# Kernel optimization log

Measured on AMD Instinct MI355X. Metric: run time of the kernel, lower is better.

## Reference

```python
import jax, jax.numpy as jnp
import numpy as np

N_NODES = 100_000
N_POS = 1_600_000
N_NEG = 1_600_000
HID = 32


def gcn_conv(x, edge_index, W, b, num_nodes):
    """torch_geometric GCNConv: add self-loops, symmetric norm, linear-first, bias after agg."""
    xl = x @ W  # [N, out]
    loops = jnp.arange(num_nodes, dtype=edge_index.dtype)
    src = jnp.concatenate([edge_index[0], loops])
    dst = jnp.concatenate([edge_index[1], loops])
    deg = jax.ops.segment_sum(jnp.ones_like(dst, dtype=xl.dtype), dst, num_segments=num_nodes)
    dinv = jnp.where(deg > 0, jax.lax.rsqrt(deg), 0.0)
    norm = dinv[src] * dinv[dst]  # [E+N]
    out = jax.ops.segment_sum(norm[:, None] * xl[src], dst, num_segments=num_nodes)
    return out + b


def setup_inputs() -> dict:
    key = jax.random.key(0)
    ks = jax.random.split(key, 8)
    x = jax.random.normal(ks[0], (N_NODES, HID), dtype=jnp.float32)
    pos_edge_index = jax.random.randint(ks[1], (2, N_POS), 0, N_NODES, dtype=jnp.int32)
    neg_edge_index = jax.random.randint(ks[2], (2, N_NEG), 0, N_NODES, dtype=jnp.int32)
    s = lambda fan_in: 1.0 / np.sqrt(fan_in)
    W1 = jax.random.normal(ks[3], (HID, 128), dtype=jnp.float32) * s(HID)
    b1 = jnp.zeros((128,), jnp.float32)
    W2 = jax.random.normal(ks[4], (128, HID), dtype=jnp.float32) * s(128)
    b2 = jnp.zeros((HID,), jnp.float32)
    Wm1 = jax.random.normal(ks[5], (2 * HID, HID), dtype=jnp.float32) * s(2 * HID)
    bm1 = jnp.zeros((HID,), jnp.float32)
    Wm2 = jax.random.normal(ks[6], (HID, 2), dtype=jnp.float32) * s(HID)
    bm2 = jnp.zeros((2,), jnp.float32)
    return dict(x=x, pos_edge_index=pos_edge_index, neg_edge_index=neg_edge_index,
                W1=W1, b1=b1, W2=W2, b2=b2, Wm1=Wm1, bm1=bm1, Wm2=Wm2, bm2=bm2)


def reference(x, pos_edge_index, neg_edge_index, W1, b1, W2, b2, Wm1, bm1, Wm2, bm2):
    n = x.shape[0]
    h = jax.nn.relu(gcn_conv(x, pos_edge_index, W1, b1, n))
    h = jax.nn.relu(gcn_conv(h, pos_edge_index, W2, b2, n))  # [N, hid]
    ei = jnp.concatenate([pos_edge_index, neg_edge_index], axis=-1)  # [2, Ep+En]
    feat = jnp.concatenate([h[ei[0]], h[ei[1]]], axis=1)  # [E, 2*hid]
    out = jax.nn.relu(feat @ Wm1 + bm1) @ Wm2 + bm2  # [E, 2]
    return out
```

## Files before the change

### kernel.cpp

```cpp
#include <hip/hip_runtime.h>
#include <hip/hip_fp16.h>


#define HIDN 32
#define SCAN_B 256

struct __align__(8) Half4 { __half2 a, b; };

__global__ void k_deg(const int* __restrict__ dst, int E, int N, int* __restrict__ deg8) {
    int e = blockIdx.x * blockDim.x + threadIdx.x;
    if (e < E)
        atomicAdd(&deg8[(size_t)(e & 7) * N + __builtin_nontemporal_load(dst + e)], 1);
}

__global__ void k_scan1(const int* __restrict__ deg8, int N,
                        int* __restrict__ part, int* __restrict__ bsum,
                        float* __restrict__ dinv,
                        const float4* __restrict__ x4, Half4* __restrict__ xs4) {
    __shared__ int sh[SCAN_B];
    __shared__ float dsh[SCAN_B];
    int t = threadIdx.x, i = blockIdx.x * SCAN_B + t;
    int v = 0;
    if (i < N) {
#pragma unroll
        for (int c = 0; c < 8; ++c) v += deg8[(size_t)c * N + i];
    }
    float dv = rsqrtf((float)(v + 1));
    if (i < N) dinv[i] = dv;
    dsh[t] = dv;
    sh[t] = v; __syncthreads();
    for (int o = 1; o < SCAN_B; o <<= 1) {
        int a = (t >= o) ? sh[t - o] : 0;
        __syncthreads();
        sh[t] += a;
        __syncthreads();
    }
    if (i < N) part[i] = sh[t] - v;
    if (t == SCAN_B - 1) bsum[blockIdx.x] = sh[t];
#pragma unroll
    for (int it = 0; it < 8; ++it) {
        int q = it * SCAN_B + t;
        int g = blockIdx.x * (SCAN_B * 8) + q;
        if (g < N * 8) {
            float w = dsh[q >> 3];
            float4 a = x4[g];
            Half4 hv;
            hv.a = __floats2half2_rn(a.x * w, a.y * w);
            hv.b = __floats2half2_rn(a.z * w, a.w * w);
            xs4[g] = hv;
        }
    }
}

__global__ void k_scan2(int* __restrict__ bsum, int nb) {
    __shared__ int sh[1024];
    int t = threadIdx.x;
    int v = (t < nb) ? bsum[t] : 0;
    sh[t] = v; __syncthreads();
    for (int o = 1; o < 1024; o <<= 1) {
        int a = (t >= o) ? sh[t - o] : 0;
        __syncthreads();
        sh[t] += a;
        __syncthreads();
    }
    if (t < nb) bsum[t] = sh[t] - v;
}

__global__ void k_scan3(const int* __restrict__ part, const int* __restrict__ bsum,
                        const int* __restrict__ deg8,
                        int N, int E, int* __restrict__ rowptr, int* __restrict__ cursor8) {
    int i = blockIdx.x * blockDim.x + threadIdx.x;
    if (i < N) {
        int r = part[i] + bsum[i / SCAN_B];
        rowptr[i] = r;
        int base = r;
#pragma unroll
        for (int c = 0; c < 8; ++c) {
            cursor8[(size_t)c * N + i] = base;
            base += deg8[(size_t)c * N + i];
        }
    }
    if (i == N) rowptr[N] = E;
}

__global__ void k_fill_sweep(const int* __restrict__ src, const int* __restrict__ dst,
                             int E, int N, int lo, int hi,
                             int* __restrict__ cursor8, int* __restrict__ csr) {
    int e = blockIdx.x * blockDim.x + threadIdx.x;
    if (e >= E) return;
    int d = __builtin_nontemporal_load(dst + e);
    if (d >= lo && d < hi) {
        int j = atomicAdd(&cursor8[(size_t)(e & 7) * N + d], 1);
        csr[j] = __builtin_nontemporal_load(src + e);
    }
}

#define ADD8(raw)                                        \
    {                                                    \
        const __half2* _h = (const __half2*)&(raw);      \
        float2 _f;                                       \
        _f = __half22float2(_h[0]); a0 += _f.x; a1 += _f.y; \
        _f = __half22float2(_h[1]); a2 += _f.x; a3 += _f.y; \
        _f = __half22float2(_h[2]); a4 += _f.x; a5 += _f.y; \
        _f = __half22float2(_h[3]); a6 += _f.x; a7 += _f.y; \
    }

__global__ void k_gather_h(const float4* __restrict__ tbl, const float* __restrict__ dinv,
                           const int* __restrict__ rowptr, const int* __restrict__ csr,
                           int N, float4* __restrict__ out) {
    int t = blockIdx.x * blockDim.x + threadIdx.x;
    if (t >= N * 4) return;
    int i = t >> 2, c = t & 3;
    float di = dinv[i];
    float a0 = 0.f, a1 = 0.f, a2 = 0.f, a3 = 0.f;
    float a4 = 0.f, a5 = 0.f, a6 = 0.f, a7 = 0.f;
    {
        float4 raw = tbl[(size_t)i * 4 + c];
        ADD8(raw);
    }
    int p = rowptr[i], end = rowptr[i + 1];
    for (; p + 3 < end; p += 4) {
        int s0 = __builtin_nontemporal_load(csr + p);
        int s1 = __builtin_nontemporal_load(csr + p + 1);
        int s2 = __builtin_nontemporal_load(csr + p + 2);
        int s3 = __builtin_nontemporal_load(csr + p + 3);
        float4 r0 = tbl[(size_t)s0 * 4 + c];
        float4 r1 = tbl[(size_t)s1 * 4 + c];
        float4 r2 = tbl[(size_t)s2 * 4 + c];
        float4 r3 = tbl[(size_t)s3 * 4 + c];
        ADD8(r0); ADD8(r1); ADD8(r2); ADD8(r3);
    }
    for (; p < end; ++p) {
        float4 r = tbl[(size_t)__builtin_nontemporal_load(csr + p) * 4 + c];
        ADD8(r);
    }
    out[(size_t)i * 8 + 2 * c]     = make_float4(a0 * di, a1 * di, a2 * di, a3 * di);
    out[(size_t)i * 8 + 2 * c + 1] = make_float4(a4 * di, a5 * di, a6 * di, a7 * di);
}

__global__ __launch_bounds__(256) void k_mlp1(
        const float4* __restrict__ agg1, const float* __restrict__ dinv,
        const float* __restrict__ W1, const float* __restrict__ b1,
        const float* __restrict__ W2, int N, __half* __restrict__ xl2s) {
    __shared__ float aT[32][65];
    __shared__ __half hT16[64][136];
    int t = threadIdx.x;
    int base = blockIdx.x * 64;
#pragma unroll
    for (int it = 0; it < 2; ++it) {
        int idx = it * 256 + t;
        int n = idx >> 3, q = idx & 7;
        int gi = base + n;
        float4 v = (gi < N) ? agg1[(size_t)gi * 8 + q] : make_float4(0.f, 0.f, 0.f, 0.f);
        aT[q * 4 + 0][n] = v.x; aT[q * 4 + 1][n] = v.y;
        aT[q * 4 + 2][n] = v.z; aT[q * 4 + 3][n] = v.w;
    }
    __syncthreads();
    int j = t & 31, r = t >> 5;
    int n0 = r * 8;
    float acc[8][4];
    {
        float4 bq = *reinterpret_cast<const float4*>(&b1[4 * j]);
#pragma unroll
        for (int n = 0; n < 8; ++n) {
            acc[n][0] = bq.x; acc[n][1] = bq.y; acc[n][2] = bq.z; acc[n][3] = bq.w;
        }
    }
#pragma unroll
    for (int k = 0; k < 32; ++k) {
        float4 w = *reinterpret_cast<const float4*>(&W1[k * 128 + 4 * j]);
#pragma unroll
        for (int n = 0; n < 8; ++n) {
            float a = aT[k][n0 + n];
            acc[n][0] = fmaf(a, w.x, acc[n][0]);
            acc[n][1] = fmaf(a, w.y, acc[n][1]);
            acc[n][2] = fmaf(a, w.z, acc[n][2]);
            acc[n][3] = fmaf(a, w.w, acc[n][3]);
        }
    }
#pragma unroll
    for (int n = 0; n < 8; ++n) {
        Half4 hv;
        hv.a = __floats2half2_rn(fmaxf(acc[n][0], 0.f), fmaxf(acc[n][1], 0.f));
        hv.b = __floats2half2_rn(fmaxf(acc[n][2], 0.f), fmaxf(acc[n][3], 0.f));
        *reinterpret_cast<Half4*>(&hT16[n0 + n][4 * j]) = hv;
    }
    __syncthreads();
    int jo = j & 7, ko = j >> 3;
    float acc2[8][4];
#pragma unroll
    for (int n = 0; n < 8; ++n) { acc2[n][0] = acc2[n][1] = acc2[n][2] = acc2[n][3] = 0.f; }
#pragma unroll
    for (int kk = 0; kk < 8; ++kk) {
        int kbase = ko * 32 + 4 * kk;
        float2 hf[8][2];
#pragma unroll
        for (int n = 0; n < 8; ++n) {
            Half4 hv = *reinterpret_cast<const Half4*>(&hT16[n0 + n][kbase]);
            hf[n][0] = __half22float2(hv.a);
            hf[n][1] = __half22float2(hv.b);
        }
#pragma unroll
        for (int c = 0; c < 4; ++c) {
            float4 w = *reinterpret_cast<const float4*>(&W2[(kbase + c) * 32 + 4 * jo]);
#pragma unroll
            for (int n = 0; n < 8; ++n) {
                float a = (c == 0) ? hf[n][0].x : (c == 1) ? hf[n][0].y
                        : (c == 2) ? hf[n][1].x : hf[n][1].y;
                acc2[n][0] = fmaf(a, w.x, acc2[n][0]);
                acc2[n][1] = fmaf(a, w.y, acc2[n][1]);
                acc2[n][2] = fmaf(a, w.z, acc2[n][2]);
                acc2[n][3] = fmaf(a, w.w, acc2[n][3]);
            }
        }
    }
#pragma unroll
    for (int n = 0; n < 8; ++n)
#pragma unroll
        for (int c = 0; c < 4; ++c) {
            acc2[n][c] += __shfl_xor(acc2[n][c], 8);
            acc2[n][c] += __shfl_xor(acc2[n][c], 16);
        }
    if (ko == 0) {
#pragma unroll
        for (int n = 0; n < 8; ++n) {
            int gi = base + n0 + n;
            if (gi < N) {
                float d = dinv[gi];
                Half4 hv;
                hv.a = __floats2half2_rn(acc2[n][0] * d, acc2[n][1] * d);
                hv.b = __floats2half2_rn(acc2[n][2] * d, acc2[n][3] * d);
                *reinterpret_cast<Half4*>(&xl2s[(size_t)gi * 32 + 4 * jo]) = hv;
            }
        }
    }
}

__global__ __launch_bounds__(256) void k_mlp2(
        const float4* __restrict__ agg2, const float* __restrict__ b2,
        const float* __restrict__ Wm1, int N,
        __half* __restrict__ gt, __half* __restrict__ gb) {
    __shared__ float hT[32][129];
    int t = threadIdx.x;
    int base = blockIdx.x * 128;
    const float4* b2q = reinterpret_cast<const float4*>(b2);
#pragma unroll
    for (int it = 0; it < 4; ++it) {
        int idx = it * 256 + t;
        int n = idx >> 3, q = idx & 7;
        int gi = base + n;
        float4 v = (gi < N) ? agg2[(size_t)gi * 8 + q] : make_float4(0.f, 0.f, 0.f, 0.f);
        float4 bb = b2q[q];
        hT[q * 4 + 0][n] = fmaxf(v.x + bb.x, 0.f);
        hT[q * 4 + 1][n] = fmaxf(v.y + bb.y, 0.f);
        hT[q * 4 + 2][n] = fmaxf(v.z + bb.z, 0.f);
        hT[q * 4 + 3][n] = fmaxf(v.w + bb.w, 0.f);
    }
    __syncthreads();
    int j = t & 15, r = t >> 4;
    int n0 = r * 8;
    int half = j >> 3, jo = j & 7;
    float acc[8][4];
#pragma unroll
    for (int n = 0; n < 8; ++n) { acc[n][0] = acc[n][1] = acc[n][2] = acc[n][3] = 0.f; }
#pragma unroll
    for (int k = 0; k < 32; ++k) {
        float4 w = *reinterpret_cast<const float4*>(&Wm1[(k + half * 32) * 32 + 4 * jo]);
#pragma unroll
        for (int n = 0; n < 8; ++n) {
            float a = hT[k][n0 + n];
            acc[n][0] = fmaf(a, w.x, acc[n][0]);
            acc[n][1] = fmaf(a, w.y, acc[n][1]);
            acc[n][2] = fmaf(a, w.z, acc[n][2]);
            acc[n][3] = fmaf(a, w.w, acc[n][3]);
        }
    }
    __half* dsttab = half ? gb : gt;
#pragma unroll
    for (int n = 0; n < 8; ++n) {
        int gi = base + n0 + n;
        if (gi < N) {
            Half4 hv;
            hv.a = __floats2half2_rn(acc[n][0], acc[n][1]);
            hv.b = __floats2half2_rn(acc[n][2], acc[n][3]);
            *reinterpret_cast<Half4*>(&dsttab[(size_t)gi * 32 + 4 * jo]) = hv;
        }
    }
}

__global__ void k_edge(const int* __restrict__ ps, const int* __restrict__ pd, int Ep,
                       const int* __restrict__ ns, const int* __restrict__ nd, int En,
                       int P,
                       const float4* __restrict__ gt4, const float4* __restrict__ gb4,
                       const float* __restrict__ bm1, const float* __restrict__ Wm2,
                       const float* __restrict__ bm2, float* __restrict__ out) {
    int t = blockIdx.x * blockDim.x + threadIdx.x;
    int p = t >> 2, q = t & 3;
    if (p >= P) return;
    int E = Ep + En;
    int e0 = p, e1 = p + P;
    int u0, v0;
    if (e0 < Ep) { u0 = __builtin_nontemporal_load(ps + e0); v0 = __builtin_nontemporal_load(pd + e0); }
    else         { u0 = __builtin_nontemporal_load(ns + (e0 - Ep)); v0 = __builtin_nontemporal_load(nd + (e0 - Ep)); }
    bool has1 = (e1 < E);
    int u1 = u0, v1 = v0;
    if (has1) {
        if (e1 < Ep) { u1 = __builtin_nontemporal_load(ps + e1); v1 = __builtin_nontemporal_load(pd + e1); }
        else         { u1 = __builtin_nontemporal_load(ns + (e1 - Ep)); v1 = __builtin_nontemporal_load(nd + (e1 - Ep)); }
    }
    float4 a0raw = gt4[(size_t)u0 * 4 + q];
    float4 b0raw = gb4[(size_t)v0 * 4 + q];
    float4 a1raw = gt4[(size_t)u1 * 4 + q];
    float4 b1raw = gb4[(size_t)v1 * 4 + q];
    const __half* a0h = (const __half*)&a0raw;
    const __half* b0h = (const __half*)&b0raw;
    const __half* a1h = (const __half*)&a1raw;
    const __half* b1h = (const __half*)&b1raw;
    int k0 = q * 8;
    float o00 = 0.f, o01 = 0.f, o10 = 0.f, o11 = 0.f;
#pragma unroll
    for (int r = 0; r < 8; ++r) {
        float bm = bm1[k0 + r];
        float w0 = Wm2[(k0 + r) * 2 + 0];
        float w1 = Wm2[(k0 + r) * 2 + 1];
        float h0 = fmaxf(__half2float(a0h[r]) + __half2float(b0h[r]) + bm, 0.f);
        o00 = fmaf(h0, w0, o00); o01 = fmaf(h0, w1, o01);
        float h1 = fmaxf(__half2float(a1h[r]) + __half2float(b1h[r]) + bm, 0.f);
        o10 = fmaf(h1, w0, o10); o11 = fmaf(h1, w1, o11);
    }
    o00 += __shfl_down(o00, 2, 4); o01 += __shfl_down(o01, 2, 4);
    o00 += __shfl_down(o00, 1, 4); o01 += __shfl_down(o01, 1, 4);
    o10 += __shfl_down(o10, 2, 4); o11 += __shfl_down(o11, 2, 4);
    o10 += __shfl_down(o10, 1, 4); o11 += __shfl_down(o11, 1, 4);
    if (q == 0) {
        float c0 = bm2[0], c1 = bm2[1];
        __builtin_nontemporal_store(o00 + c0, out + (size_t)e0 * 2 + 0);
        __builtin_nontemporal_store(o01 + c1, out + (size_t)e0 * 2 + 1);
        if (has1) {
            __builtin_nontemporal_store(o10 + c0, out + (size_t)e1 * 2 + 0);
            __builtin_nontemporal_store(o11 + c1, out + (size_t)e1 * 2 + 1);
        }
    }
}

extern "C" void kernel_launch(void* const* d_in, const int* in_sizes, int n_in,
                              void* d_out, int out_size, void* d_ws, size_t ws_size,
                              hipStream_t stream) {
    const float* x   = (const float*)d_in[0];
    const int*   pei = (const int*)d_in[1];
    const int*   nei = (const int*)d_in[2];
    const float* W1  = (const float*)d_in[3];
    const float* b1  = (const float*)d_in[4];
    const float* W2  = (const float*)d_in[5];
    const float* b2  = (const float*)d_in[6];
    const float* Wm1 = (const float*)d_in[7];
    const float* bm1 = (const float*)d_in[8];
    const float* Wm2 = (const float*)d_in[9];
    const float* bm2 = (const float*)d_in[10];

    const int N  = in_sizes[0] / HIDN;
    const int Ep = in_sizes[1] / 2;
    const int En = in_sizes[2] / 2;
    const int* ps = pei;
    const int* pd = pei + Ep;
    const int* ns = nei;
    const int* nd = nei + En;
    const int nb = (N + SCAN_B - 1) / SCAN_B;

    char* ws = (char*)d_ws;
    size_t off = 0;
    auto alloc = [&](size_t bytes) { size_t o = off; off += (bytes + 255) & ~(size_t)255; return o; };
    int*    deg8    = (int*)(ws + alloc((size_t)N * 8 * 4));
    int*    cursor8 = (int*)(ws + alloc((size_t)N * 8 * 4));
    float*  dinv    = (float*)(ws + alloc((size_t)N * 4));
    int*    part    = (int*)(ws + alloc((size_t)N * 4));
    int*    bsum    = (int*)(ws + alloc((size_t)1024 * 4));
    int*    rowptr  = (int*)(ws + alloc((size_t)(N + 1) * 4));
    int*    csr     = (int*)(ws + alloc((size_t)Ep * 4));
    __half* xs      = (__half*)(ws + alloc((size_t)N * HIDN * 2));
    float*  agg1    = (float*)(ws + alloc((size_t)N * HIDN * 4));
    __half* xl2s    = (__half*)(ws + alloc((size_t)N * HIDN * 2));
    float*  agg2    = (float*)(ws + alloc((size_t)N * HIDN * 4));
    __half* gt      = (__half*)(ws + alloc((size_t)N * HIDN * 2));
    __half* gb      = (__half*)(ws + alloc((size_t)N * HIDN * 2));

    hipMemsetAsync(deg8, 0, (size_t)N * 8 * 4, stream);
    k_deg<<<(Ep + 255) / 256, 256, 0, stream>>>(pd, Ep, N, deg8);
    k_scan1<<<nb, SCAN_B, 0, stream>>>(deg8, N, part, bsum, dinv,
                                       (const float4*)x, (Half4*)xs);
    k_scan2<<<1, 1024, 0, stream>>>(bsum, nb);
    k_scan3<<<(N + 256) / 256, 256, 0, stream>>>(part, bsum, deg8, N, Ep, rowptr, cursor8);
    {
        int grid = (Ep + 255) / 256;
        for (int s = 0; s < 4; ++s) {
            int lo = (int)((size_t)N * s / 4);
            int hi = (int)((size_t)N * (s + 1) / 4);
            k_fill_sweep<<<grid, 256, 0, stream>>>(ps, pd, Ep, N, lo, hi, cursor8, csr);
        }
    }

    k_gather_h<<<(N * 4 + 255) / 256, 256, 0, stream>>>(
        (const float4*)xs, dinv, rowptr, csr, N, (float4*)agg1);
    k_mlp1<<<(N + 63) / 64, 256, 0, stream>>>(
        (const float4*)agg1, dinv, W1, b1, W2, N, xl2s);

    k_gather_h<<<(N * 4 + 255) / 256, 256, 0, stream>>>(
        (const float4*)xl2s, dinv, rowptr, csr, N, (float4*)agg2);
    k_mlp2<<<(N + 127) / 128, 256, 0, stream>>>(
        (const float4*)agg2, b2, Wm1, N, gt, gb);

    {
        int E = Ep + En;
        int P = (E + 1) / 2;
        size_t threads = (size_t)P * 4;
        k_edge<<<(int)((threads + 255) / 256), 256, 0, stream>>>(
            ps, pd, Ep, ns, nd, En, P,
            (const float4*)gt, (const float4*)gb,
            bm1, Wm2, bm2, (float*)d_out);
    }
}
```

Before: 362.5 us.

## Fuse CSR gather into per-layer MLP kernels and split edge kernel in halves

The neighbor gather is folded into both dense layer kernels. Each block aggregates its 64 nodes directly into shared memory, so the fp32 agg1/agg2 intermediates are no longer written to and read back from global memory. The second layer's tile shrinks from 128 to 64 nodes so the gather maps one node per four threads. The edge MLP kernel is also launched as two half-range chunks. This removes two launches and about 25 MB of global traffic per layer. In exchange, the irregular gather now shares a block with the FMA work, which may cost occupancy and latency hiding.

```diff
diff --git a/kernel.cpp b/kernel.cpp
--- a/kernel.cpp
+++ b/kernel.cpp
@@ -105,55 +105,50 @@
         _f = __half22float2(_h[3]); a6 += _f.x; a7 += _f.y; \
     }
 
-__global__ void k_gather_h(const float4* __restrict__ tbl, const float* __restrict__ dinv,
-                           const int* __restrict__ rowptr, const int* __restrict__ csr,
-                           int N, float4* __restrict__ out) {
-    int t = blockIdx.x * blockDim.x + threadIdx.x;
-    if (t >= N * 4) return;
-    int i = t >> 2, c = t & 3;
-    float di = dinv[i];
-    float a0 = 0.f, a1 = 0.f, a2 = 0.f, a3 = 0.f;
-    float a4 = 0.f, a5 = 0.f, a6 = 0.f, a7 = 0.f;
-    {
-        float4 raw = tbl[(size_t)i * 4 + c];
-        ADD8(raw);
-    }
-    int p = rowptr[i], end = rowptr[i + 1];
-    for (; p + 3 < end; p += 4) {
-        int s0 = __builtin_nontemporal_load(csr + p);
-        int s1 = __builtin_nontemporal_load(csr + p + 1);
-        int s2 = __builtin_nontemporal_load(csr + p + 2);
-        int s3 = __builtin_nontemporal_load(csr + p + 3);
-        float4 r0 = tbl[(size_t)s0 * 4 + c];
-        float4 r1 = tbl[(size_t)s1 * 4 + c];
-        float4 r2 = tbl[(size_t)s2 * 4 + c];
-        float4 r3 = tbl[(size_t)s3 * 4 + c];
-        ADD8(r0); ADD8(r1); ADD8(r2); ADD8(r3);
-    }
-    for (; p < end; ++p) {
-        float4 r = tbl[(size_t)__builtin_nontemporal_load(csr + p) * 4 + c];
-        ADD8(r);
-    }
-    out[(size_t)i * 8 + 2 * c]     = make_float4(a0 * di, a1 * di, a2 * di, a3 * di);
-    out[(size_t)i * 8 + 2 * c + 1] = make_float4(a4 * di, a5 * di, a6 * di, a7 * di);
-}
-
-__global__ __launch_bounds__(256) void k_mlp1(
-        const float4* __restrict__ agg1, const float* __restrict__ dinv,
+__global__ __launch_bounds__(256) void k_l1(
+        const float4* __restrict__ xs, const float* __restrict__ dinv,
+        const int* __restrict__ rowptr, const int* __restrict__ csr,
         const float* __restrict__ W1, const float* __restrict__ b1,
         const float* __restrict__ W2, int N, __half* __restrict__ xl2s) {
     __shared__ float aT[32][65];
     __shared__ __half hT16[64][136];
     int t = threadIdx.x;
     int base = blockIdx.x * 64;
-#pragma unroll
-    for (int it = 0; it < 2; ++it) {
-        int idx = it * 256 + t;
-        int n = idx >> 3, q = idx & 7;
+    {
+        int n = t >> 2, c = t & 3;
         int gi = base + n;
-        float4 v = (gi < N) ? agg1[(size_t)gi * 8 + q] : make_float4(0.f, 0.f, 0.f, 0.f);
-        aT[q * 4 + 0][n] = v.x; aT[q * 4 + 1][n] = v.y;
-        aT[q * 4 + 2][n] = v.z; aT[q * 4 + 3][n] = v.w;
+        float a0 = 0.f, a1 = 0.f, a2 = 0.f, a3 = 0.f;
+        float a4 = 0.f, a5 = 0.f, a6 = 0.f, a7 = 0.f;
+        if (gi < N) {
+            float di = dinv[gi];
+            {
+                float4 raw = xs[(size_t)gi * 4 + c];
+                ADD8(raw);
+            }
+            int p = rowptr[gi], end = rowptr[gi + 1];
+            for (; p + 3 < end; p += 4) {
+                int s0 = __builtin_nontemporal_load(csr + p);
+                int s1 = __builtin_nontemporal_load(csr + p + 1);
+                int s2 = __builtin_nontemporal_load(csr + p + 2);
+                int s3 = __builtin_nontemporal_load(csr + p + 3);
+                float4 r0 = xs[(size_t)s0 * 4 + c];
+                float4 r1 = xs[(size_t)s1 * 4 + c];
+                float4 r2 = xs[(size_t)s2 * 4 + c];
+                float4 r3 = xs[(size_t)s3 * 4 + c];
+                ADD8(r0); ADD8(r1); ADD8(r2); ADD8(r3);
+            }
+            for (; p < end; ++p) {
+                float4 rr = xs[(size_t)__builtin_nontemporal_load(csr + p) * 4 + c];
+                ADD8(rr);
+            }
+            a0 *= di; a1 *= di; a2 *= di; a3 *= di;
+            a4 *= di; a5 *= di; a6 *= di; a7 *= di;
+        }
+        int f0 = c * 8;
+        aT[f0 + 0][n] = a0; aT[f0 + 1][n] = a1;
+        aT[f0 + 2][n] = a2; aT[f0 + 3][n] = a3;
+        aT[f0 + 4][n] = a4; aT[f0 + 5][n] = a5;
+        aT[f0 + 6][n] = a6; aT[f0 + 7][n] = a7;
     }
     __syncthreads();
     int j = t & 31, r = t >> 5;
@@ -236,38 +231,66 @@
     }
 }
 
-__global__ __launch_bounds__(256) void k_mlp2(
-        const float4* __restrict__ agg2, const float* __restrict__ b2,
-        const float* __restrict__ Wm1, int N,
-        __half* __restrict__ gt, __half* __restrict__ gb) {
-    __shared__ float hT[32][129];
+__global__ __launch_bounds__(256) void k_l2(
+        const float4* __restrict__ xl2s, const float* __restrict__ dinv,
+        const int* __restrict__ rowptr, const int* __restrict__ csr,
+        const float* __restrict__ b2, const float* __restrict__ Wm1,
+        int N, __half* __restrict__ gt, __half* __restrict__ gb) {
+    __shared__ float hT[32][65];
     int t = threadIdx.x;
-    int base = blockIdx.x * 128;
-    const float4* b2q = reinterpret_cast<const float4*>(b2);
-#pragma unroll
-    for (int it = 0; it < 4; ++it) {
-        int idx = it * 256 + t;
-        int n = idx >> 3, q = idx & 7;
+    int base = blockIdx.x * 64;
+    {
+        int n = t >> 2, c = t & 3;
         int gi = base + n;
-        float4 v = (gi < N) ? agg2[(size_t)gi * 8 + q] : make_float4(0.f, 0.f, 0.f, 0.f);
-        float4 bb = b2q[q];
-        hT[q * 4 + 0][n] = fmaxf(v.x + bb.x, 0.f);
-        hT[q * 4 + 1][n] = fmaxf(v.y + bb.y, 0.f);
-        hT[q * 4 + 2][n] = fmaxf(v.z + bb.z, 0.f);
-        hT[q * 4 + 3][n] = fmaxf(v.w + bb.w, 0.f);
+        float a0 = 0.f, a1 = 0.f, a2 = 0.f, a3 = 0.f;
+        float a4 = 0.f, a5 = 0.f, a6 = 0.f, a7 = 0.f;
+        float di = 0.f;
+        if (gi < N) {
+            di = dinv[gi];
+            {
+                float4 raw = xl2s[(size_t)gi * 4 + c];
+                ADD8(raw);
+            }
+            int p = rowptr[gi], end = rowptr[gi + 1];
+            for (; p + 3 < end; p += 4) {
+                int s0 = __builtin_nontemporal_load(csr + p);
+                int s1 = __builtin_nontemporal_load(csr + p + 1);
+                int s2 = __builtin_nontemporal_load(csr + p + 2);
+                int s3 = __builtin_nontemporal_load(csr + p + 3);
+                float4 r0 = xl2s[(size_t)s0 * 4 + c];
+                float4 r1 = xl2s[(size_t)s1 * 4 + c];
+                float4 r2 = xl2s[(size_t)s2 * 4 + c];
+                float4 r3 = xl2s[(size_t)s3 * 4 + c];
+                ADD8(r0); ADD8(r1); ADD8(r2); ADD8(r3);
+            }
+            for (; p < end; ++p) {
+                float4 rr = xl2s[(size_t)__builtin_nontemporal_load(csr + p) * 4 + c];
+                ADD8(rr);
+            }
+        }
+        int f0 = c * 8;
+        const float* bb = b2 + f0;
+        hT[f0 + 0][n] = fmaxf(fmaf(a0, di, bb[0]), 0.f);
+        hT[f0 + 1][n] = fmaxf(fmaf(a1, di, bb[1]), 0.f);
+        hT[f0 + 2][n] = fmaxf(fmaf(a2, di, bb[2]), 0.f);
+        hT[f0 + 3][n] = fmaxf(fmaf(a3, di, bb[3]), 0.f);
+        hT[f0 + 4][n] = fmaxf(fmaf(a4, di, bb[4]), 0.f);
+        hT[f0 + 5][n] = fmaxf(fmaf(a5, di, bb[5]), 0.f);
+        hT[f0 + 6][n] = fmaxf(fmaf(a6, di, bb[6]), 0.f);
+        hT[f0 + 7][n] = fmaxf(fmaf(a7, di, bb[7]), 0.f);
     }
     __syncthreads();
     int j = t & 15, r = t >> 4;
-    int n0 = r * 8;
+    int n0 = r * 4;
     int half = j >> 3, jo = j & 7;
-    float acc[8][4];
-#pragma unroll
-    for (int n = 0; n < 8; ++n) { acc[n][0] = acc[n][1] = acc[n][2] = acc[n][3] = 0.f; }
+    float acc[4][4];
+#pragma unroll
+    for (int n = 0; n < 4; ++n) { acc[n][0] = acc[n][1] = acc[n][2] = acc[n][3] = 0.f; }
 #pragma unroll
     for (int k = 0; k < 32; ++k) {
         float4 w = *reinterpret_cast<const float4*>(&Wm1[(k + half * 32) * 32 + 4 * jo]);
 #pragma unroll
-        for (int n = 0; n < 8; ++n) {
+        for (int n = 0; n < 4; ++n) {
             float a = hT[k][n0 + n];
             acc[n][0] = fmaf(a, w.x, acc[n][0]);
             acc[n][1] = fmaf(a, w.y, acc[n][1]);
@@ -277,7 +300,7 @@
     }
     __half* dsttab = half ? gb : gt;
 #pragma unroll
-    for (int n = 0; n < 8; ++n) {
+    for (int n = 0; n < 4; ++n) {
         int gi = base + n0 + n;
         if (gi < N) {
             Half4 hv;
@@ -290,19 +313,20 @@
 
 __global__ void k_edge(const int* __restrict__ ps, const int* __restrict__ pd, int Ep,
                        const int* __restrict__ ns, const int* __restrict__ nd, int En,
-                       int P,
+                       int elo, int ehi,
                        const float4* __restrict__ gt4, const float4* __restrict__ gb4,
                        const float* __restrict__ bm1, const float* __restrict__ Wm2,
                        const float* __restrict__ bm2, float* __restrict__ out) {
     int t = blockIdx.x * blockDim.x + threadIdx.x;
     int p = t >> 2, q = t & 3;
-    if (p >= P) return;
-    int E = Ep + En;
-    int e0 = p, e1 = p + P;
+    int cnt = ehi - elo;
+    int Pc = (cnt + 1) >> 1;
+    if (p >= Pc) return;
+    int e0 = elo + p, e1 = elo + p + Pc;
     int u0, v0;
     if (e0 < Ep) { u0 = __builtin_nontemporal_load(ps + e0); v0 = __builtin_nontemporal_load(pd + e0); }
     else         { u0 = __builtin_nontemporal_load(ns + (e0 - Ep)); v0 = __builtin_nontemporal_load(nd + (e0 - Ep)); }
-    bool has1 = (e1 < E);
+    bool has1 = (e1 < ehi);
     int u1 = u0, v1 = v0;
     if (has1) {
         if (e1 < Ep) { u1 = __builtin_nontemporal_load(ps + e1); v1 = __builtin_nontemporal_load(pd + e1); }
@@ -378,9 +402,7 @@
     int*    rowptr  = (int*)(ws + alloc((size_t)(N + 1) * 4));
     int*    csr     = (int*)(ws + alloc((size_t)Ep * 4));
     __half* xs      = (__half*)(ws + alloc((size_t)N * HIDN * 2));
-    float*  agg1    = (float*)(ws + alloc((size_t)N * HIDN * 4));
     __half* xl2s    = (__half*)(ws + alloc((size_t)N * HIDN * 2));
-    float*  agg2    = (float*)(ws + alloc((size_t)N * HIDN * 4));
     __half* gt      = (__half*)(ws + alloc((size_t)N * HIDN * 2));
     __half* gb      = (__half*)(ws + alloc((size_t)N * HIDN * 2));
 
@@ -399,23 +421,23 @@
         }
     }
 
-    k_gather_h<<<(N * 4 + 255) / 256, 256, 0, stream>>>(
-        (const float4*)xs, dinv, rowptr, csr, N, (float4*)agg1);
-    k_mlp1<<<(N + 63) / 64, 256, 0, stream>>>(
-        (const float4*)agg1, dinv, W1, b1, W2, N, xl2s);
-
-    k_gather_h<<<(N * 4 + 255) / 256, 256, 0, stream>>>(
-        (const float4*)xl2s, dinv, rowptr, csr, N, (float4*)agg2);
-    k_mlp2<<<(N + 127) / 128, 256, 0, stream>>>(
-        (const float4*)agg2, b2, Wm1, N, gt, gb);
+    k_l1<<<(N + 63) / 64, 256, 0, stream>>>(
+        (const float4*)xs, dinv, rowptr, csr, W1, b1, W2, N, xl2s);
+    k_l2<<<(N + 63) / 64, 256, 0, stream>>>(
+        (const float4*)xl2s, dinv, rowptr, csr, b2, Wm1, N, gt, gb);
 
     {
         int E = Ep + En;
-        int P = (E + 1) / 2;
-        size_t threads = (size_t)P * 4;
-        k_edge<<<(int)((threads + 255) / 256), 256, 0, stream>>>(
-            ps, pd, Ep, ns, nd, En, P,
-            (const float4*)gt, (const float4*)gb,
-            bm1, Wm2, bm2, (float*)d_out);
-    }
-}
+        for (int c = 0; c < 2; ++c) {
+            int elo = (int)((size_t)E * c / 2);
+            int ehi = (int)((size_t)E * (c + 1) / 2);
+            int cnt = ehi - elo;
+            int Pc = (cnt + 1) / 2;
+            size_t threads = (size_t)Pc * 4;
+            k_edge<<<(int)((threads + 255) / 256), 256, 0, stream>>>(
+                ps, pd, Ep, ns, nd, En, elo, ehi,
+                (const float4*)gt, (const float4*)gb,
+                bm1, Wm2, bm2, (float*)d_out);
+        }
+    }
+}
```

New measurement: 383.4 us. 1.06x slower.
